# Kernel optimization log

Measured on AMD Instinct MI355X. Metric: run time of the kernel, lower is better.

The kernel has to match this reference:

```python
import jax, jax.numpy as jnp
import numpy as np

SIZE = 128   # feature dim
N = 4096     # number of mesh nodes


def setup_inputs() -> dict:
    key = jax.random.key(0)
    k_f, k_adj, k_q, k_k = jax.random.split(key, 4)
    # f: [size, N] node features (features-first, as in the torch module); scaled
    # so QK dot products stay O(1) and exp() is numerically safe.
    f = jax.random.normal(k_f, (SIZE, N), dtype=jnp.float32) * 0.1
    # neighbors: [N, N] binary adjacency with self-loops (every row sums > 0).
    adj = (jax.random.uniform(k_adj, (N, N)) < 0.005).astype(jnp.float32)
    neighbors = jnp.maximum(adj, jnp.eye(N, dtype=jnp.float32))
    # learned per-feature scale vectors (nn.init.normal_)
    wq = jax.random.normal(k_q, (SIZE,), dtype=jnp.float32)
    wk = jax.random.normal(k_k, (SIZE,), dtype=jnp.float32)
    return {"f": f, "neighbors": neighbors, "wq": wq, "wk": wk}


def reference(f, neighbors, wq, wk):
    # elementwise-scaled queries/keys: [size, N]
    wq_f = wq[:, None] * f
    wk_f = wk[:, None] * f
    # S[i, j] = exp(<wq_f[:, i], wk_f[:, j]>)  -> [N, N]
    S = jnp.exp(jnp.einsum('dn,dm->nm', wq_f, wk_f))
    # normalize by neighbor-sums: S / (neighbors @ S).T
    S = S / jnp.matmul(neighbors, S).T
    return S
```

## Files before the change

### kernel.cpp

```cpp
#include <hip/hip_runtime.h>
#include <hip/hip_fp16.h>

#define N    4096
#define SIZE 128
#define CAP  128
#define RB   16
#define TB   1024
#define SW   256

typedef __attribute__((ext_vector_type(8))) _Float16 f16x8;
typedef __attribute__((ext_vector_type(2))) __fp16 fp16x2;
typedef __attribute__((ext_vector_type(4))) float f32x4;

__device__ __forceinline__ unsigned int pk2(float lo, float hi) {
    union { fp16x2 v; unsigned int u; } c;
    c.v = __builtin_amdgcn_cvt_pkrtz(lo, hi);
    return c.u;
}
__device__ __forceinline__ __half2 u2h(unsigned int u) {
    union { unsigned int u; __half2 h; } c; c.u = u; return c.h;
}

__global__ __launch_bounds__(256)
void build_csr(const float* __restrict__ nb, int* __restrict__ cnt4,
               int* __restrict__ idx) {
    __shared__ int sc;
    const int j    = blockIdx.x;
    const int lane = threadIdx.x & 63;
    if (threadIdx.x == 0) sc = 0;
    __syncthreads();
    const float4* row4 = (const float4*)(nb + (size_t)j * N);
    int* irow = idx + (size_t)j * CAP;

    float4 v[4];
#pragma unroll
    for (int it = 0; it < 4; ++it) v[it] = row4[threadIdx.x + it * 256];

#pragma unroll
    for (int it = 0; it < 4; ++it) {
        const float e[4] = {v[it].x, v[it].y, v[it].z, v[it].w};
#pragma unroll
        for (int q = 0; q < 4; ++q) {
            const bool nz = (e[q] != 0.0f);
            const unsigned long long m = __ballot(nz);
            if (m != 0ull) {
                int base = 0;
                if (lane == 0) base = atomicAdd(&sc, __popcll(m));
                base = __shfl(base, 0);
                if (nz) {
                    const int p = base + __popcll(m & ((1ull << lane) - 1ull));
                    const int c = 4 * (threadIdx.x + it * 256) + q;
                    if (p < CAP) irow[p] = c;
                }
            }
        }
    }
    __syncthreads();
    if (threadIdx.x == 0) {
        int n  = (sc < CAP) ? sc : CAP;
        int n4 = (n + 3) & ~3;
        for (int p = n; p < n4; ++p) irow[p] = N;
        cnt4[j] = n4 >> 2;
    }
}

__global__ __launch_bounds__(SW)
void sortw(const int* __restrict__ cnt4, int* __restrict__ perm) {
    __shared__ int hist[65];
    __shared__ int ofs[65];
    const int w = blockIdx.x, t = threadIdx.x;
    if (t < 65) hist[t] = 0;
    __syncthreads();
    const int j = w * SW + t;
    int k = cnt4[j]; if (k > 64) k = 64;
    atomicAdd(&hist[k], 1);
    __syncthreads();
    if (t == 0) {
        int s = 0;
        for (int b = 0; b <= 64; ++b) { ofs[b] = s; s += hist[b]; }
    }
    __syncthreads();
    const int pos = atomicAdd(&ofs[k], 1);
    perm[w * SW + pos] = j;
}

__global__ __launch_bounds__(256)
void prep(const float* __restrict__ f, const float* __restrict__ wq,
          const float* __restrict__ wk, _Float16* __restrict__ Af,
          _Float16* __restrict__ Bf) {
    __shared__ float sf[SIZE][16];
    __shared__ float sqw[SIZE];
    const int t    = threadIdx.x;
    const int tile = blockIdx.x;
    if (t < SIZE) sqw[t] = wq[t] * wk[t];
    const int col0 = t & 15;
#pragma unroll
    for (int it = 0; it < 8; ++it) {
        const int k = (t >> 4) + it * 16;
        sf[k][col0] = f[(size_t)k * N + tile * 16 + col0];
    }
    __syncthreads();

    const int ks   = t >> 6;
    const int lane = t & 63;
    const int quad = lane >> 4;
    const int col  = lane & 15;
    f16x8 va, vb;
#pragma unroll
    for (int jj = 0; jj < 8; ++jj) {
        const int k = ks * 32 + quad * 8 + jj;
        const float v = sf[k][col];
        va[jj] = (_Float16)(sqw[k] * v);
        vb[jj] = (_Float16)v;
    }
    const size_t o = (size_t)(tile * 4 + ks) * 64 + lane;
    ((f16x8*)Af)[o] = va;
    ((f16x8*)Bf)[o] = vb;
}

__global__ __launch_bounds__(TB, 4)
void fused(const _Float16* __restrict__ Af, const _Float16* __restrict__ Bf,
           const int* __restrict__ cnt4, const int* __restrict__ idx,
           const int* __restrict__ perm, float* __restrict__ out) {
    __shared__ uint4 Sb[2 * N + 3];
    uint4* const sA = Sb;
    uint4* const sB = Sb + N + 2;
    const int t    = threadIdx.x;
    const int lane = t & 63;
    const int wv   = t >> 6;
    const int quad = lane >> 4;
    const int i0   = blockIdx.x * RB;

    f16x8 af[4];
    const f16x8* Ap = (const f16x8*)Af + (size_t)blockIdx.x * 4 * 64;
#pragma unroll
    for (int ks = 0; ks < 4; ++ks) af[ks] = Ap[ks * 64 + lane];
    const f16x8* Bp = (const f16x8*)Bf;

#pragma unroll 4
    for (int ti = 0; ti < 16; ++ti) {
        const int nt = wv * 16 + ti;
        f32x4 acc = {0.f, 0.f, 0.f, 0.f};
#pragma unroll
        for (int ks = 0; ks < 4; ++ks) {
            const f16x8 bfrag = Bp[(size_t)(nt * 4 + ks) * 64 + lane];
            acc = __builtin_amdgcn_mfma_f32_16x16x32_f16(af[ks], bfrag, acc, 0, 0, 0);
        }
        const int j = nt * 16 + (lane & 15);
        uint2 p;
        p.x = pk2(__expf(acc[0]), __expf(acc[1]));
        p.y = pk2(__expf(acc[2]), __expf(acc[3]));
        uint2* base = (quad < 2) ? (uint2*)&sA[j] : (uint2*)&sB[j];
        base[quad & 1] = p;
    }
    if (t == 0) {
        sA[N] = make_uint4(0u, 0u, 0u, 0u);
        sB[N] = make_uint4(0u, 0u, 0u, 0u);
    }
    __syncthreads();

    for (int u = 0; u < N / TB; ++u) {
        const int jp = perm[t + u * TB];
        const int c4 = cnt4[jp];
        const int4* irow = (const int4*)(idx + (size_t)jp * CAP);
        __half2 d0[8], d1[8];
        const __half2 z = u2h(0u);
#pragma unroll
        for (int r = 0; r < 8; ++r) { d0[r] = z; d1[r] = z; }

        int4 k = irow[0];
        for (int c = 0; c < c4; ++c) {
            const int4 kn = (c + 1 < c4) ? irow[c + 1] : k;
            const uint4 ax = sA[k.x], bx = sB[k.x];
            const uint4 ay = sA[k.y], by = sB[k.y];
            const uint4 az = sA[k.z], bz = sB[k.z];
            const uint4 aw = sA[k.w], bw = sB[k.w];
            d0[0] = __hadd2(d0[0], u2h(ax.x)); d1[0] = __hadd2(d1[0], u2h(ay.x));
            d0[1] = __hadd2(d0[1], u2h(ax.y)); d1[1] = __hadd2(d1[1], u2h(ay.y));
            d0[2] = __hadd2(d0[2], u2h(ax.z)); d1[2] = __hadd2(d1[2], u2h(ay.z));
            d0[3] = __hadd2(d0[3], u2h(ax.w)); d1[3] = __hadd2(d1[3], u2h(ay.w));
            d0[4] = __hadd2(d0[4], u2h(bx.x)); d1[4] = __hadd2(d1[4], u2h(by.x));
            d0[5] = __hadd2(d0[5], u2h(bx.y)); d1[5] = __hadd2(d1[5], u2h(by.y));
            d0[6] = __hadd2(d0[6], u2h(bx.z)); d1[6] = __hadd2(d1[6], u2h(by.z));
            d0[7] = __hadd2(d0[7], u2h(bx.w)); d1[7] = __hadd2(d1[7], u2h(by.w));
            d0[0] = __hadd2(d0[0], u2h(az.x)); d1[0] = __hadd2(d1[0], u2h(aw.x));
            d0[1] = __hadd2(d0[1], u2h(az.y)); d1[1] = __hadd2(d1[1], u2h(aw.y));
            d0[2] = __hadd2(d0[2], u2h(az.z)); d1[2] = __hadd2(d1[2], u2h(aw.z));
            d0[3] = __hadd2(d0[3], u2h(az.w)); d1[3] = __hadd2(d1[3], u2h(aw.w));
            d0[4] = __hadd2(d0[4], u2h(bz.x)); d1[4] = __hadd2(d1[4], u2h(bw.x));
            d0[5] = __hadd2(d0[5], u2h(bz.y)); d1[5] = __hadd2(d1[5], u2h(bw.y));
            d0[6] = __hadd2(d0[6], u2h(bz.z)); d1[6] = __hadd2(d1[6], u2h(bw.z));
            d0[7] = __hadd2(d0[7], u2h(bz.w)); d1[7] = __hadd2(d1[7], u2h(bw.w));
            k = kn;
        }
        const uint4 na = sA[jp], nb2 = sB[jp];
        const unsigned int nu[8] = {na.x, na.y, na.z, na.w, nb2.x, nb2.y, nb2.z, nb2.w};
#pragma unroll
        for (int i = 0; i < 8; ++i) {
            const __half2 dd = __hadd2(d0[i], d1[i]);
            const __half2 nn = u2h(nu[i]);
            out[(size_t)(i0 + 2 * i + 0) * N + jp] =
                __low2float(nn)  * __builtin_amdgcn_rcpf(__low2float(dd));
            out[(size_t)(i0 + 2 * i + 1) * N + jp] =
                __high2float(nn) * __builtin_amdgcn_rcpf(__high2float(dd));
        }
    }
}

extern "C" void kernel_launch(void* const* d_in, const int* in_sizes, int n_in,
                              void* d_out, int out_size, void* d_ws, size_t ws_size,
                              hipStream_t stream) {
    const float* f  = (const float*)d_in[0];
    const float* nb = (const float*)d_in[1];
    const float* wq = (const float*)d_in[2];
    const float* wk = (const float*)d_in[3];
    float* out = (float*)d_out;

    int*      cnt4 = (int*)d_ws;
    int*      idx  = cnt4 + N;
    int*      perm = idx + (size_t)N * CAP;
    _Float16* Af   = (_Float16*)(perm + N);
    _Float16* Bf   = Af + (size_t)256 * 4 * 64 * 8;

    build_csr<<<N, 256, 0, stream>>>(nb, cnt4, idx);
    sortw<<<N / SW, SW, 0, stream>>>(cnt4, perm);
    prep<<<256, 256, 0, stream>>>(f, wq, wk, Af, Bf);
    fused<<<N / RB, TB, 0, stream>>>(Af, Bf, cnt4, idx, perm, out);
}
```

Baseline: 181.6 us.

## Stage permuted outputs in LDS for coalesced stores and drop CSR padding

Each thread's permuted output column is written into a shared staging buffer as packed half2 values, then written back to global memory in natural column order, so stores become coalesced instead of scattered by the sort permutation. The CSR build no longer pads to multiples of four with a sentinel; a scalar tail loop handles the remainder, and the sort histogram uses exact counts. The cost is 32KB of extra LDS, two block barriers per output chunk, and output values rounded to fp16 before the fp32 write, which loses precision. Launch bounds drop to one block per CU, which matches the LDS now in use.

```diff
diff --git a/kernel.cpp b/kernel.cpp
--- a/kernel.cpp
+++ b/kernel.cpp
@@ -22,7 +22,7 @@
 }
 
 __global__ __launch_bounds__(256)
-void build_csr(const float* __restrict__ nb, int* __restrict__ cnt4,
+void build_csr(const float* __restrict__ nb, int* __restrict__ cnt,
                int* __restrict__ idx) {
     __shared__ int sc;
     const int j    = blockIdx.x;
@@ -56,28 +56,23 @@
         }
     }
     __syncthreads();
-    if (threadIdx.x == 0) {
-        int n  = (sc < CAP) ? sc : CAP;
-        int n4 = (n + 3) & ~3;
-        for (int p = n; p < n4; ++p) irow[p] = N;
-        cnt4[j] = n4 >> 2;
-    }
+    if (threadIdx.x == 0) cnt[j] = (sc < CAP) ? sc : CAP;
 }
 
 __global__ __launch_bounds__(SW)
-void sortw(const int* __restrict__ cnt4, int* __restrict__ perm) {
-    __shared__ int hist[65];
-    __shared__ int ofs[65];
+void sortw(const int* __restrict__ cnt, int* __restrict__ perm) {
+    __shared__ int hist[128];
+    __shared__ int ofs[128];
     const int w = blockIdx.x, t = threadIdx.x;
-    if (t < 65) hist[t] = 0;
+    if (t < 128) hist[t] = 0;
     __syncthreads();
     const int j = w * SW + t;
-    int k = cnt4[j]; if (k > 64) k = 64;
+    int k = cnt[j]; if (k > 127) k = 127;
     atomicAdd(&hist[k], 1);
     __syncthreads();
     if (t == 0) {
         int s = 0;
-        for (int b = 0; b <= 64; ++b) { ofs[b] = s; s += hist[b]; }
+        for (int b = 0; b < 128; ++b) { ofs[b] = s; s += hist[b]; }
     }
     __syncthreads();
     const int pos = atomicAdd(&ofs[k], 1);
@@ -118,13 +113,14 @@
     ((f16x8*)Bf)[o] = vb;
 }
 
-__global__ __launch_bounds__(TB, 4)
+__global__ __launch_bounds__(TB, 1)
 void fused(const _Float16* __restrict__ Af, const _Float16* __restrict__ Bf,
-           const int* __restrict__ cnt4, const int* __restrict__ idx,
+           const int* __restrict__ cnt, const int* __restrict__ idx,
            const int* __restrict__ perm, float* __restrict__ out) {
-    __shared__ uint4 Sb[2 * N + 3];
+    __shared__ uint4 Sb[2 * N];
+    __shared__ unsigned int stg[8][TB];
     uint4* const sA = Sb;
-    uint4* const sB = Sb + N + 2;
+    uint4* const sB = Sb + N;
     const int t    = threadIdx.x;
     const int lane = t & 63;
     const int wv   = t >> 6;
@@ -153,57 +149,75 @@
         uint2* base = (quad < 2) ? (uint2*)&sA[j] : (uint2*)&sB[j];
         base[quad & 1] = p;
     }
-    if (t == 0) {
-        sA[N] = make_uint4(0u, 0u, 0u, 0u);
-        sB[N] = make_uint4(0u, 0u, 0u, 0u);
-    }
     __syncthreads();
 
     for (int u = 0; u < N / TB; ++u) {
         const int jp = perm[t + u * TB];
-        const int c4 = cnt4[jp];
-        const int4* irow = (const int4*)(idx + (size_t)jp * CAP);
+        const int n  = cnt[jp];
+        const int c4 = n >> 2;
+        const int* irow = idx + (size_t)jp * CAP;
+        const int4* irow4 = (const int4*)irow;
         __half2 d0[8], d1[8];
         const __half2 z = u2h(0u);
 #pragma unroll
         for (int r = 0; r < 8; ++r) { d0[r] = z; d1[r] = z; }
 
-        int4 k = irow[0];
-        for (int c = 0; c < c4; ++c) {
-            const int4 kn = (c + 1 < c4) ? irow[c + 1] : k;
-            const uint4 ax = sA[k.x], bx = sB[k.x];
-            const uint4 ay = sA[k.y], by = sB[k.y];
-            const uint4 az = sA[k.z], bz = sB[k.z];
-            const uint4 aw = sA[k.w], bw = sB[k.w];
-            d0[0] = __hadd2(d0[0], u2h(ax.x)); d1[0] = __hadd2(d1[0], u2h(ay.x));
-            d0[1] = __hadd2(d0[1], u2h(ax.y)); d1[1] = __hadd2(d1[1], u2h(ay.y));
-            d0[2] = __hadd2(d0[2], u2h(ax.z)); d1[2] = __hadd2(d1[2], u2h(ay.z));
-            d0[3] = __hadd2(d0[3], u2h(ax.w)); d1[3] = __hadd2(d1[3], u2h(ay.w));
-            d0[4] = __hadd2(d0[4], u2h(bx.x)); d1[4] = __hadd2(d1[4], u2h(by.x));
-            d0[5] = __hadd2(d0[5], u2h(bx.y)); d1[5] = __hadd2(d1[5], u2h(by.y));
-            d0[6] = __hadd2(d0[6], u2h(bx.z)); d1[6] = __hadd2(d1[6], u2h(by.z));
-            d0[7] = __hadd2(d0[7], u2h(bx.w)); d1[7] = __hadd2(d1[7], u2h(by.w));
-            d0[0] = __hadd2(d0[0], u2h(az.x)); d1[0] = __hadd2(d1[0], u2h(aw.x));
-            d0[1] = __hadd2(d0[1], u2h(az.y)); d1[1] = __hadd2(d1[1], u2h(aw.y));
-            d0[2] = __hadd2(d0[2], u2h(az.z)); d1[2] = __hadd2(d1[2], u2h(aw.z));
-            d0[3] = __hadd2(d0[3], u2h(az.w)); d1[3] = __hadd2(d1[3], u2h(aw.w));
-            d0[4] = __hadd2(d0[4], u2h(bz.x)); d1[4] = __hadd2(d1[4], u2h(bw.x));
-            d0[5] = __hadd2(d0[5], u2h(bz.y)); d1[5] = __hadd2(d1[5], u2h(bw.y));
-            d0[6] = __hadd2(d0[6], u2h(bz.z)); d1[6] = __hadd2(d1[6], u2h(bw.z));
-            d0[7] = __hadd2(d0[7], u2h(bz.w)); d1[7] = __hadd2(d1[7], u2h(bw.w));
-            k = kn;
-        }
+        if (c4 > 0) {
+            int4 k = irow4[0];
+            for (int c = 0; c < c4; ++c) {
+                const int4 kn = (c + 1 < c4) ? irow4[c + 1] : k;
+                const uint4 ax = sA[k.x], bx = sB[k.x];
+                const uint4 ay = sA[k.y], by = sB[k.y];
+                const uint4 az = sA[k.z], bz = sB[k.z];
+                const uint4 aw = sA[k.w], bw = sB[k.w];
+                d0[0] = __hadd2(d0[0], u2h(ax.x)); d1[0] = __hadd2(d1[0], u2h(ay.x));
+                d0[1] = __hadd2(d0[1], u2h(ax.y)); d1[1] = __hadd2(d1[1], u2h(ay.y));
+                d0[2] = __hadd2(d0[2], u2h(ax.z)); d1[2] = __hadd2(d1[2], u2h(ay.z));
+                d0[3] = __hadd2(d0[3], u2h(ax.w)); d1[3] = __hadd2(d1[3], u2h(ay.w));
+                d0[4] = __hadd2(d0[4], u2h(bx.x)); d1[4] = __hadd2(d1[4], u2h(by.x));
+                d0[5] = __hadd2(d0[5], u2h(bx.y)); d1[5] = __hadd2(d1[5], u2h(by.y));
+                d0[6] = __hadd2(d0[6], u2h(bx.z)); d1[6] = __hadd2(d1[6], u2h(by.z));
+                d0[7] = __hadd2(d0[7], u2h(bx.w)); d1[7] = __hadd2(d1[7], u2h(by.w));
+                d0[0] = __hadd2(d0[0], u2h(az.x)); d1[0] = __hadd2(d1[0], u2h(aw.x));
+                d0[1] = __hadd2(d0[1], u2h(az.y)); d1[1] = __hadd2(d1[1], u2h(aw.y));
+                d0[2] = __hadd2(d0[2], u2h(az.z)); d1[2] = __hadd2(d1[2], u2h(aw.z));
+                d0[3] = __hadd2(d0[3], u2h(az.w)); d1[3] = __hadd2(d1[3], u2h(aw.w));
+                d0[4] = __hadd2(d0[4], u2h(bz.x)); d1[4] = __hadd2(d1[4], u2h(bw.x));
+                d0[5] = __hadd2(d0[5], u2h(bz.y)); d1[5] = __hadd2(d1[5], u2h(bw.y));
+                d0[6] = __hadd2(d0[6], u2h(bz.z)); d1[6] = __hadd2(d1[6], u2h(bw.z));
+                d0[7] = __hadd2(d0[7], u2h(bz.w)); d1[7] = __hadd2(d1[7], u2h(bw.w));
+                k = kn;
+            }
+        }
+        for (int m = 4 * c4; m < n; ++m) {
+            const int kk = irow[m];
+            const uint4 a = sA[kk], b = sB[kk];
+            d0[0] = __hadd2(d0[0], u2h(a.x)); d0[1] = __hadd2(d0[1], u2h(a.y));
+            d0[2] = __hadd2(d0[2], u2h(a.z)); d0[3] = __hadd2(d0[3], u2h(a.w));
+            d0[4] = __hadd2(d0[4], u2h(b.x)); d0[5] = __hadd2(d0[5], u2h(b.y));
+            d0[6] = __hadd2(d0[6], u2h(b.z)); d0[7] = __hadd2(d0[7], u2h(b.w));
+        }
+
         const uint4 na = sA[jp], nb2 = sB[jp];
         const unsigned int nu[8] = {na.x, na.y, na.z, na.w, nb2.x, nb2.y, nb2.z, nb2.w};
+        const int jl = jp & (TB - 1);
 #pragma unroll
         for (int i = 0; i < 8; ++i) {
             const __half2 dd = __hadd2(d0[i], d1[i]);
             const __half2 nn = u2h(nu[i]);
-            out[(size_t)(i0 + 2 * i + 0) * N + jp] =
-                __low2float(nn)  * __builtin_amdgcn_rcpf(__low2float(dd));
-            out[(size_t)(i0 + 2 * i + 1) * N + jp] =
-                __high2float(nn) * __builtin_amdgcn_rcpf(__high2float(dd));
-        }
+            const float lo = __low2float(nn)  * __builtin_amdgcn_rcpf(__low2float(dd));
+            const float hi = __high2float(nn) * __builtin_amdgcn_rcpf(__high2float(dd));
+            stg[i][jl] = pk2(lo, hi);
+        }
+        __syncthreads();
+        const int j = t + u * TB;
+#pragma unroll
+        for (int i = 0; i < 8; ++i) {
+            const __half2 o2 = u2h(stg[i][t]);
+            out[(size_t)(i0 + 2 * i + 0) * N + j] = __low2float(o2);
+            out[(size_t)(i0 + 2 * i + 1) * N + j] = __high2float(o2);
+        }
+        __syncthreads();
     }
 }
 
@@ -216,14 +230,14 @@
     const float* wk = (const float*)d_in[3];
     float* out = (float*)d_out;
 
-    int*      cnt4 = (int*)d_ws;
-    int*      idx  = cnt4 + N;
+    int*      cnt  = (int*)d_ws;
+    int*      idx  = cnt + N;
     int*      perm = idx + (size_t)N * CAP;
     _Float16* Af   = (_Float16*)(perm + N);
     _Float16* Bf   = Af + (size_t)256 * 4 * 64 * 8;
 
-    build_csr<<<N, 256, 0, stream>>>(nb, cnt4, idx);
-    sortw<<<N / SW, SW, 0, stream>>>(cnt4, perm);
+    build_csr<<<N, 256, 0, stream>>>(nb, cnt, idx);
+    sortw<<<N / SW, SW, 0, stream>>>(cnt, perm);
     prep<<<256, 256, 0, stream>>>(f, wq, wk, Af, Bf);
-    fused<<<N / RB, TB, 0, stream>>>(Af, Bf, cnt4, idx, perm, out);
-}
+    fused<<<N / RB, TB, 0, stream>>>(Af, Bf, cnt, idx, perm, out);
+}
```

New measurement: 177.1 us. 1.03x faster.
